# Kernel tuning notes

Measured on AMD Instinct MI355X. Metric: run time of the kernel, lower is better.

## Reference

```python
import jax, jax.numpy as jnp
import numpy as np

H = 16  # num_heads

def _rotate_half(x):
    x1, x2 = jnp.split(x, 2, axis=-1)
    return jnp.concatenate((-x2, x1), axis=-1)

def setup_inputs() -> dict:
    key = jax.random.key(0)
    ks = jax.random.split(key, 8)
    B, N, C = 4, 2048, 1024
    d = C // H
    x = jax.random.normal(ks[0], (B, N, C), dtype=jnp.float32)
    cos = jax.random.uniform(ks[1], (1, 1, N, d), dtype=jnp.float32)
    sin = jax.random.uniform(ks[2], (1, 1, N, d), dtype=jnp.float32)
    s = 0.02
    Wq = jax.random.normal(ks[3], (C, C), dtype=jnp.float32) * s
    Wkv = jax.random.normal(ks[4], (C, 2 * C), dtype=jnp.float32) * s
    Wout = jax.random.normal(ks[5], (C, C), dtype=jnp.float32) * s
    bout = jnp.zeros((C,), dtype=jnp.float32)
    return {"x": x, "cos": cos, "sin": sin, "Wq": Wq, "Wkv": Wkv, "Wout": Wout, "bout": bout}

def reference(x, cos, sin, Wq, Wkv, Wout, bout):
    B, N, C = x.shape
    d = C // H
    scale = d ** (-0.5)
    # projections (qkv_bias=False)
    q = (x @ Wq).reshape(B, N, H, d).transpose(0, 2, 1, 3)        # (B,H,N,d)
    kv = x @ Wkv                                                   # (B,N,2C)
    k, v = jnp.split(kv, 2, axis=-1)
    k = k.reshape(B, N, H, d).transpose(0, 2, 1, 3)
    v = v.reshape(B, N, H, d).transpose(0, 2, 1, 3)
    # inline RoPE
    q = q * cos + _rotate_half(q) * sin
    k = k * cos + _rotate_half(k) * sin
    # naive full attention
    sim = jnp.einsum('bhid,bhjd->bhij', q, k) * scale              # (B,H,N,N)
    attn = jax.nn.softmax(sim, axis=-1)
    out = jnp.einsum('bhij,bhjd->bhid', attn, v)                   # (B,H,N,d)
    out = out.transpose(0, 2, 1, 3).reshape(B, N, C)
    return out @ Wout + bout
```

## Files before the change

kernel.cpp:

```cpp
#include <hip/hip_runtime.h>


typedef unsigned short u16;
typedef unsigned int u32;
typedef __attribute__((ext_vector_type(8))) short short8;
typedef __attribute__((ext_vector_type(8))) unsigned short ushort8;
typedef __attribute__((ext_vector_type(4))) float f32x4;

#define MFMA16x16x32 __builtin_amdgcn_mfma_f32_16x16x32_bf16
#define QSCALE 0.180336880434135f

#if __has_builtin(__builtin_amdgcn_exp2f)
#define EXP2F __builtin_amdgcn_exp2f
#else
#define EXP2F exp2f
#endif

__device__ __forceinline__ float b2f(u16 u) {
  union { u32 i; float f; } x; x.i = ((u32)u) << 16; return x.f;
}
__device__ __forceinline__ u16 f2b(float f) {
  union { float f; u32 i; } x; x.f = f;
  u32 r = (x.i + 0x7FFFu + ((x.i >> 16) & 1u)) >> 16;
  return (u16)r;
}
__device__ __forceinline__ u16 f2b_trunc(float f) {
  union { float f; u32 i; } x; x.f = f;
  return (u16)(x.i >> 16);
}
__device__ __forceinline__ bool detect_f32(const u32* __restrict__ cw) {
  u32 acc = 0;
#pragma unroll
  for (int i = 0; i < 64; ++i) acc |= cw[i];
  return (acc & 0x8000u) != 0;
}
__device__ __forceinline__ float ldval(const void* p, long i, bool f32) {
  return f32 ? ((const float*)p)[i] : b2f(((const u16*)p)[i]);
}
__device__ __forceinline__ ushort8 ld8f(const float* p) {
  float4 u0 = *(const float4*)p;
  float4 u1 = *(const float4*)(p + 4);
  ushort8 r;
  r[0] = f2b(u0.x); r[1] = f2b(u0.y); r[2] = f2b(u0.z); r[3] = f2b(u0.w);
  r[4] = f2b(u1.x); r[5] = f2b(u1.y); r[6] = f2b(u1.z); r[7] = f2b(u1.w);
  return r;
}
__device__ __forceinline__ void async16(const void* g, void* l) {
  __builtin_amdgcn_global_load_lds((const __attribute__((address_space(1))) void*)g,
                                   (__attribute__((address_space(3))) void*)l, 16, 0, 0);
}

__global__ __launch_bounds__(256)
void convert_x(const void* __restrict__ src, u16* __restrict__ dst,
               const u32* __restrict__ cosw) {
  const bool f32 = detect_f32(cosw);
  const long i = ((long)blockIdx.x * 256 + threadIdx.x) * 8;
  ushort8 v;
  if (f32) v = ld8f((const float*)src + i);
  else     v = *(const ushort8*)((const u16*)src + i);
  *(ushort8*)(dst + i) = v;
}

__global__ __launch_bounds__(256)
void transpose_any(const void* __restrict__ src, u16* __restrict__ dst,
                   int R, int C, const u32* __restrict__ cosw) {
  const bool f32 = detect_f32(cosw);
  const int tr = blockIdx.y * 64, tc = blockIdx.x * 64;
  __shared__ __align__(16) u16 tile[64][65];
  const int t = threadIdx.x;
#pragma unroll
  for (int i = 0; i < 2; ++i) {
    const int ch = i * 256 + t;
    const int r = ch >> 3, cc = ch & 7;
    ushort8 v;
    if (f32) v = ld8f((const float*)src + (long)(tr + r) * C + tc + cc * 8);
    else     v = *(const ushort8*)((const u16*)src + (long)(tr + r) * C + tc + cc * 8);
#pragma unroll
    for (int j = 0; j < 8; ++j) tile[r][cc * 8 + j] = v[j];
  }
  __syncthreads();
#pragma unroll
  for (int i = 0; i < 2; ++i) {
    const int ch = i * 256 + t;
    const int c = ch >> 3, rc = ch & 7;
    ushort8 v;
#pragma unroll
    for (int j = 0; j < 8; ++j) v[j] = tile[rc * 8 + j][c];
    *(ushort8*)(dst + (long)(tc + c) * R + tr + rc * 8) = v;
  }
}

__global__ __launch_bounds__(256)
void transpose_b16(const u16* __restrict__ src, u16* __restrict__ dst,
                   int R, int C, long sb, long db) {
  src += (long)blockIdx.z * sb;
  dst += (long)blockIdx.z * db;
  const int tr = blockIdx.y * 64, tc = blockIdx.x * 64;
  __shared__ __align__(16) u16 tile[64][65];
  const int t = threadIdx.x;
#pragma unroll
  for (int i = 0; i < 2; ++i) {
    const int ch = i * 256 + t;
    const int r = ch >> 3, cc = ch & 7;
    ushort8 v = *(const ushort8*)(src + (long)(tr + r) * C + tc + cc * 8);
#pragma unroll
    for (int j = 0; j < 8; ++j) tile[r][cc * 8 + j] = v[j];
  }
  __syncthreads();
#pragma unroll
  for (int i = 0; i < 2; ++i) {
    const int ch = i * 256 + t;
    const int c = ch >> 3, rc = ch & 7;
    ushort8 v;
#pragma unroll
    for (int j = 0; j < 8; ++j) v[j] = tile[rc * 8 + j][c];
    *(ushort8*)(dst + (long)(tc + c) * R + tr + rc * 8) = v;
  }
}

template <int MODE>
__global__ __launch_bounds__(256)
void gemm_fast(const u16* __restrict__ A, const u16* __restrict__ BT,
               const void* cosp, const void* sinp,
               u16* q_ws, u16* k_ws, u16* v_ws,
               const void* bias, void* outp, const u32* __restrict__ cosw) {
  constexpr int K = 1024, ITERS = K / 32;
  __shared__ __align__(16) u16 As[2][128 * 32];
  __shared__ __align__(16) u16 Bs[2][128 * 32];
  const int tid = threadIdx.x;
  const int wave = tid >> 6, lane = tid & 63;
  const int quad = lane >> 4, l15 = lane & 15;
  const int m0 = blockIdx.y * 128, n0 = blockIdx.x * 128;
  const int mh = (wave >> 1) * 64, nh = (wave & 1) * 64;
  const f32x4 zero4 = {0.f, 0.f, 0.f, 0.f};

  f32x4 acc[4][4];
#pragma unroll
  for (int i = 0; i < 4; ++i)
#pragma unroll
    for (int j = 0; j < 4; ++j) acc[i][j] = zero4;

  const int c0 = tid, c1 = 256 + tid;
  const u16* a0p = A  + (long)(m0 + (c0 >> 2)) * K + (c0 & 3) * 8;
  const u16* a1p = A  + (long)(m0 + (c1 >> 2)) * K + (c1 & 3) * 8;
  const u16* b0p = BT + (long)(n0 + (c0 >> 2)) * K + (c0 & 3) * 8;
  const u16* b1p = BT + (long)(n0 + (c1 >> 2)) * K + (c1 & 3) * 8;

#define STAGE(buf, kt)                                \
  do {                                                \
    async16(a0p + (kt), As[buf] + c0 * 8);            \
    async16(a1p + (kt), As[buf] + c1 * 8);            \
    async16(b0p + (kt), Bs[buf] + c0 * 8);            \
    async16(b1p + (kt), Bs[buf] + c1 * 8);            \
  } while (0)

  STAGE(0, 0);
  for (int it = 0; it < ITERS; ++it) {
    const int cur = it & 1;
    __syncthreads();
    if (it + 1 < ITERS) STAGE(cur ^ 1, (it + 1) * 32);
    short8 af[4], bf[4];
#pragma unroll
    for (int s = 0; s < 4; ++s) {
      af[s] = *(const short8*)(As[cur] + (mh + s * 16 + l15) * 32 + quad * 8);
      bf[s] = *(const short8*)(Bs[cur] + (nh + s * 16 + l15) * 32 + quad * 8);
    }
#pragma unroll
    for (int i = 0; i < 4; ++i)
#pragma unroll
      for (int j = 0; j < 4; ++j)
        acc[i][j] = MFMA16x16x32(af[i], bf[j], acc[i][j], 0, 0, 0);
  }
#undef STAGE

  const bool f32 = detect_f32(cosw);

  if (MODE == 0) {
    const int seg = n0 >> 10;
    const int csbase = (n0 & 1023) + nh;
    u16* segp = (seg == 0) ? q_ws : (seg == 1) ? k_ws : v_ws;
#pragma unroll
    for (int i = 0; i < 4; ++i) {
#pragma unroll
      for (int r = 0; r < 4; ++r) {
        const int mm = m0 + mh + i * 16 + quad * 4 + r;
        const int b = mm >> 11, n = mm & 2047;
#pragma unroll
        for (int j = 0; j < 4; ++j) {
          const int cs = csbase + j * 16 + l15;
          const int h = cs >> 6, dv = cs & 63;
          float val = acc[i][j][r];
          if (seg < 2) {
            const float cv = ldval(cosp, (long)n * 64 + dv, f32);
            const float sv = ldval(sinp, (long)n * 64 + dv, f32);
            const float part = acc[i][j ^ 2][r];
            val = val * cv + ((dv < 32) ? -part : part) * sv;
            if (seg == 0) val *= QSCALE;
          }
          segp[(((long)(b * 16 + h) * 2048 + n) << 6) + dv] = f2b(val);
        }
      }
    }
  } else {
#pragma unroll
    for (int i = 0; i < 4; ++i) {
#pragma unroll
      for (int r = 0; r < 4; ++r) {
        const int mm = m0 + mh + i * 16 + quad * 4 + r;
#pragma unroll
        for (int j = 0; j < 4; ++j) {
          const int cc = n0 + nh + j * 16 + l15;
          const float val = acc[i][j][r] + ldval(bias, cc, f32);
          if (f32) ((float*)outp)[(long)mm * 1024 + cc] = val;
          else     ((u16*)outp)[(long)mm * 1024 + cc] = f2b(val);
        }
      }
    }
  }
}

__global__ __launch_bounds__(256)
void flash_k(const u16* __restrict__ q_ws, const u16* __restrict__ k_ws,
             const u16* __restrict__ vT_ws, u16* __restrict__ attn) {
  __shared__ __align__(16) u16 Ks[2][64 * 64];
  __shared__ __align__(16) u16 Vts[2][64 * 64];
  __shared__ __align__(16) u16 Pw[4][64 * 40];
  const int tid = threadIdx.x, wave = tid >> 6, lane = tid & 63;
  const int quad = lane >> 4, l15 = lane & 15;
  const int s7 = l15 & 7;
  const int bh = blockIdx.y;
  const int qr0 = blockIdx.x * 256 + wave * 64;
  const u16* Q  = q_ws  + (long)bh * 2048 * 64;
  const u16* Kp = k_ws  + (long)bh * 2048 * 64;
  const u16* Vt = vT_ws + (long)bh * 64 * 2048;
  u16* Pb = Pw[wave];
  const f32x4 zero4 = {0.f, 0.f, 0.f, 0.f};
  short8 ones;
#pragma unroll
  for (int i = 0; i < 8; ++i) ones[i] = (short)0x3F80;

  short8 aq[4][2];
#pragma unroll
  for (int ms = 0; ms < 4; ++ms)
#pragma unroll
    for (int ks = 0; ks < 2; ++ks)
      aq[ms][ks] = *(const short8*)(Q + (long)(qr0 + ms * 16 + l15) * 64 + ks * 32 + quad * 8);

  f32x4 accO[4][4], accL[4];
#pragma unroll
  for (int ms = 0; ms < 4; ++ms) {
#pragma unroll
    for (int jd = 0; jd < 4; ++jd) accO[ms][jd] = zero4;
    accL[ms] = zero4;
  }

  const int c0 = tid, c1 = 256 + tid;
  const int r0 = c0 >> 3, g0 = ((c0 & 7) ^ (r0 & 7)) * 8;
  const int r1 = c1 >> 3, g1 = ((c1 & 7) ^ (r1 & 7)) * 8;

#define STAGEKV(buf, kt)                                          \
  do {                                                            \
    async16(Kp + (long)((kt) + r0) * 64 + g0, Ks[buf] + c0 * 8);  \
    async16(Kp + (long)((kt) + r1) * 64 + g1, Ks[buf] + c1 * 8);  \
    async16(Vt + (long)r0 * 2048 + (kt) + g0, Vts[buf] + c0 * 8); \
    async16(Vt + (long)r1 * 2048 + (kt) + g1, Vts[buf] + c1 * 8); \
  } while (0)

  STAGEKV(0, 0);
  for (int it = 0; it < 32; ++it) {
    const int cur = it & 1;
    __syncthreads();
    if (it + 1 < 32) STAGEKV(cur ^ 1, (it + 1) * 64);

#pragma unroll
    for (int k2 = 0; k2 < 2; ++k2) {
#pragma unroll
      for (int nsl = 0; nsl < 2; ++nsl) {
        const int ns = k2 * 2 + nsl;
        const u16* rowK = Ks[cur] + (ns * 16 + l15) * 64;
        short8 b0 = *(const short8*)(rowK + ((quad ^ s7) * 8));
        short8 b1 = *(const short8*)(rowK + (((quad + 4) ^ s7) * 8));
#pragma unroll
        for (int ms = 0; ms < 4; ++ms) {
          f32x4 t = MFMA16x16x32(aq[ms][0], b0, zero4, 0, 0, 0);
          f32x4 sa = MFMA16x16x32(aq[ms][1], b1, t, 0, 0, 0);
#pragma unroll
          for (int r = 0; r < 4; ++r)
            Pb[(ms * 16 + quad * 4 + r) * 40 + nsl * 16 + l15] =
                f2b_trunc(EXP2F(sa[r]));
        }
      }
      short8 ap[4];
#pragma unroll
      for (int ms = 0; ms < 4; ++ms) {
        ap[ms] = *(const short8*)(Pb + (ms * 16 + l15) * 40 + quad * 8);
        accL[ms] = MFMA16x16x32(ap[ms], ones, accL[ms], 0, 0, 0);
      }
#pragma unroll
      for (int jd = 0; jd < 4; ++jd) {
        short8 bv = *(const short8*)(Vts[cur] + (jd * 16 + l15) * 64 +
                                     (((k2 * 4 + quad) ^ s7) * 8));
#pragma unroll
        for (int ms = 0; ms < 4; ++ms)
          accO[ms][jd] = MFMA16x16x32(ap[ms], bv, accO[ms][jd], 0, 0, 0);
      }
    }
  }
#undef STAGEKV

  const int b = bh >> 4, h = bh & 15;
#pragma unroll
  for (int ms = 0; ms < 4; ++ms) {
#pragma unroll
    for (int r = 0; r < 4; ++r) {
      const float inv = 1.f / accL[ms][r];
      const int row = qr0 + ms * 16 + quad * 4 + r;
#pragma unroll
      for (int jd = 0; jd < 4; ++jd) {
        const int cc = h * 64 + jd * 16 + l15;
        attn[((long)(b * 2048 + row)) * 1024 + cc] = f2b(accO[ms][jd][r] * inv);
      }
    }
  }
}

extern "C" void kernel_launch(void* const* d_in, const int* in_sizes, int n_in,
                              void* d_out, int out_size, void* d_ws, size_t ws_size,
                              hipStream_t stream) {
  const void* x    = d_in[0];
  const void* cosp = d_in[1];
  const void* sinp = d_in[2];
  const void* Wq   = d_in[3];
  const void* Wkv  = d_in[4];
  const void* Wout = d_in[5];
  const void* bout = d_in[6];
  const u32* cosw  = (const u32*)d_in[1];

  char* ws = (char*)d_ws;
  const size_t MB = 1u << 20;
  u16* q_ws  = (u16*)(ws);
  u16* k_ws  = (u16*)(ws + 16 * MB);
  u16* vT_ws = (u16*)(ws + 32 * MB);
  u16* v_ws  = (u16*)(ws + 48 * MB);
  u16* attn  = (u16*)(ws + 48 * MB);
  u16* WoutT = (u16*)(ws + 32 * MB);

  u16* WT1;
  if (ws_size >= 88 * MB) WT1 = (u16*)(ws + 64 * MB);
  else                    WT1 = (u16*)d_out;
  u16* x_bf16 = WT1 + 3072 * 1024;

  convert_x<<<dim3(4096), 256, 0, stream>>>(x, x_bf16, cosw);
  transpose_any<<<dim3(16, 16), 256, 0, stream>>>(Wq, WT1, 1024, 1024, cosw);
  transpose_any<<<dim3(32, 16), 256, 0, stream>>>(Wkv, WT1 + 1024 * 1024, 1024, 2048, cosw);
  gemm_fast<0><<<dim3(24, 64), 256, 0, stream>>>(x_bf16, WT1, cosp, sinp,
                                                 q_ws, k_ws, v_ws,
                                                 nullptr, nullptr, cosw);
  transpose_b16<<<dim3(1, 32, 64), 256, 0, stream>>>(v_ws, vT_ws, 2048, 64,
                                                     (long)2048 * 64, (long)64 * 2048);
  flash_k<<<dim3(8, 64), 256, 0, stream>>>(q_ws, k_ws, vT_ws, attn);
  transpose_any<<<dim3(16, 16), 256, 0, stream>>>(Wout, WoutT, 1024, 1024, cosw);
  gemm_fast<1><<<dim3(8, 64), 256, 0, stream>>>(attn, WoutT, cosp, sinp,
                                                nullptr, nullptr, nullptr,
                                                bout, d_out, cosw);
}
```

Measured before the change: 344.1 us.

## Replace 128x128 GEMM with 256x256-tile 8-wave pipelined GEMM using swizzled LDS

The projection and output GEMMs move from 128x128 tiles with 256 threads to 256x256 tiles with 512 threads and a K-step of 64. LDS uses an XOR swizzle to avoid bank conflicts, and global loads are staged in quarter-chunks interleaved with MFMA phases, using explicit vmcnt waits, barriers and setprio. Workgroup indices are remapped for L2 locality. The intent is more data reuse per LDS load and better overlap of loads with compute. The cost is fewer workgroups (128 for the output GEMM, which may underfill the CUs), more registers, and a fragile hand-written synchronisation scheme.

```diff
diff --git a/kernel.cpp b/kernel.cpp
--- a/kernel.cpp
+++ b/kernel.cpp
@@ -15,6 +15,10 @@
 #else
 #define EXP2F exp2f
 #endif
+
+#define GBAR() __builtin_amdgcn_s_barrier()
+#define CFENCE() asm volatile("" ::: "memory")
+#define WAITVM(n) asm volatile("s_waitcnt vmcnt(" #n ")" ::: "memory")
 
 __device__ __forceinline__ float b2f(u16 u) {
   union { u32 i; float f; } x; x.i = ((u32)u) << 16; return x.f;
@@ -119,71 +123,160 @@
 }
 
 template <int MODE>
-__global__ __launch_bounds__(256)
-void gemm_fast(const u16* __restrict__ A, const u16* __restrict__ BT,
-               const void* cosp, const void* sinp,
-               u16* q_ws, u16* k_ws, u16* v_ws,
-               const void* bias, void* outp, const u32* __restrict__ cosw) {
-  constexpr int K = 1024, ITERS = K / 32;
-  __shared__ __align__(16) u16 As[2][128 * 32];
-  __shared__ __align__(16) u16 Bs[2][128 * 32];
+__global__ __launch_bounds__(512, 2)
+void gemm256(const u16* __restrict__ A, const u16* __restrict__ BT,
+             const void* cosp, const void* sinp,
+             u16* q_ws, u16* k_ws, u16* v_ws,
+             const void* bias, void* outp, const u32* __restrict__ cosw) {
+  constexpr int K = 1024, NT = K / 64;
+  constexpr int NB = (MODE == 0) ? 12 : 4;
+  __shared__ __align__(16) u16 As[2][16384];
+  __shared__ __align__(16) u16 Bs[2][16384];
+
   const int tid = threadIdx.x;
   const int wave = tid >> 6, lane = tid & 63;
   const int quad = lane >> 4, l15 = lane & 15;
-  const int m0 = blockIdx.y * 128, n0 = blockIdx.x * 128;
-  const int mh = (wave >> 1) * 64, nh = (wave & 1) * 64;
+  const int wr = wave >> 2, wc = wave & 3;
+  const int s7 = l15 & 7;
+
+  int lin = blockIdx.y * NB + blockIdx.x;
+  const int nwg = NB * 32;
+  lin = (lin & 7) * (nwg >> 3) + (lin >> 3);
+  const int bx = lin % NB, by = lin / NB;
+  const int m0 = by * 256, n0 = bx * 256;
+
+  const long aoff = (long)(tid >> 3) * K + (long)(((tid & 7) ^ ((tid >> 3) & 7)) * 8);
+  const u16* Ag = A  + (long)m0 * K + aoff;
+  const u16* Bg = BT + (long)n0 * K + aoff;
+
+#define STAGE_A(bb, kt, h) do {                                                          \
+    async16(Ag + (long)(2 * (h))     * 64 * K + (kt) * 64,                               \
+            As[bb] + ((2 * (h))     * 512 + tid) * 8);                                   \
+    async16(Ag + (long)(2 * (h) + 1) * 64 * K + (kt) * 64,                               \
+            As[bb] + ((2 * (h) + 1) * 512 + tid) * 8);                                   \
+  } while (0)
+#define STAGE_B(bb, kt, h) do {                                                          \
+    async16(Bg + (long)(2 * (h))     * 64 * K + (kt) * 64,                               \
+            Bs[bb] + ((2 * (h))     * 512 + tid) * 8);                                   \
+    async16(Bg + (long)(2 * (h) + 1) * 64 * K + (kt) * 64,                               \
+            Bs[bb] + ((2 * (h) + 1) * 512 + tid) * 8);                                   \
+  } while (0)
+
+  const int kg0 = (quad ^ s7) * 8;
+  const int kg1 = ((quad + 4) ^ s7) * 8;
+  const int rowA = (wr * 128 + l15) * 64;
+  const int rowB = (wc * 64 + l15) * 64;
+
   const f32x4 zero4 = {0.f, 0.f, 0.f, 0.f};
-
-  f32x4 acc[4][4];
-#pragma unroll
-  for (int i = 0; i < 4; ++i)
+  f32x4 acc[8][4];
+#pragma unroll
+  for (int i = 0; i < 8; ++i)
 #pragma unroll
     for (int j = 0; j < 4; ++j) acc[i][j] = zero4;
 
-  const int c0 = tid, c1 = 256 + tid;
-  const u16* a0p = A  + (long)(m0 + (c0 >> 2)) * K + (c0 & 3) * 8;
-  const u16* a1p = A  + (long)(m0 + (c1 >> 2)) * K + (c1 & 3) * 8;
-  const u16* b0p = BT + (long)(n0 + (c0 >> 2)) * K + (c0 & 3) * 8;
-  const u16* b1p = BT + (long)(n0 + (c1 >> 2)) * K + (c1 & 3) * 8;
-
-#define STAGE(buf, kt)                                \
-  do {                                                \
-    async16(a0p + (kt), As[buf] + c0 * 8);            \
-    async16(a1p + (kt), As[buf] + c1 * 8);            \
-    async16(b0p + (kt), Bs[buf] + c0 * 8);            \
-    async16(b1p + (kt), Bs[buf] + c1 * 8);            \
-  } while (0)
-
-  STAGE(0, 0);
-  for (int it = 0; it < ITERS; ++it) {
-    const int cur = it & 1;
-    __syncthreads();
-    if (it + 1 < ITERS) STAGE(cur ^ 1, (it + 1) * 32);
-    short8 af[4], bf[4];
-#pragma unroll
-    for (int s = 0; s < 4; ++s) {
-      af[s] = *(const short8*)(As[cur] + (mh + s * 16 + l15) * 32 + quad * 8);
-      bf[s] = *(const short8*)(Bs[cur] + (nh + s * 16 + l15) * 32 + quad * 8);
-    }
+  STAGE_B(0, 0, 0);
+  STAGE_A(0, 0, 0);
+  STAGE_A(0, 0, 1);
+  STAGE_B(0, 0, 1);
+  STAGE_B(1, 1, 0);
+  WAITVM(2);
+  GBAR(); CFENCE();
+
+#pragma unroll 2
+  for (int t = 0; t < NT; ++t) {
+    const int buf = t & 1;
+    const u16* Ab = As[buf] + rowA;
+    const u16* Bb = Bs[buf] + rowB;
+    short8 a0[4][2], a1[4][2], b01[2][2], b23[2][2];
+
+#pragma unroll
+    for (int i = 0; i < 4; ++i) {
+      a0[i][0] = *(const short8*)(Ab + i * 1024 + kg0);
+      a0[i][1] = *(const short8*)(Ab + i * 1024 + kg1);
+    }
+#pragma unroll
+    for (int j = 0; j < 2; ++j) {
+      b01[j][0] = *(const short8*)(Bb + j * 1024 + kg0);
+      b01[j][1] = *(const short8*)(Bb + j * 1024 + kg1);
+    }
+    if (t + 1 < NT) STAGE_A(buf ^ 1, t + 1, 0);
+    GBAR();
+    __builtin_amdgcn_s_setprio(1);
 #pragma unroll
     for (int i = 0; i < 4; ++i)
 #pragma unroll
-      for (int j = 0; j < 4; ++j)
-        acc[i][j] = MFMA16x16x32(af[i], bf[j], acc[i][j], 0, 0, 0);
-  }
-#undef STAGE
+      for (int j = 0; j < 2; ++j) {
+        acc[i][j] = MFMA16x16x32(a0[i][0], b01[j][0], acc[i][j], 0, 0, 0);
+        acc[i][j] = MFMA16x16x32(a0[i][1], b01[j][1], acc[i][j], 0, 0, 0);
+      }
+    __builtin_amdgcn_s_setprio(0);
+    GBAR();
+
+#pragma unroll
+    for (int i = 0; i < 4; ++i) {
+      a1[i][0] = *(const short8*)(Ab + (4 + i) * 1024 + kg0);
+      a1[i][1] = *(const short8*)(Ab + (4 + i) * 1024 + kg1);
+    }
+    if (t + 1 < NT) STAGE_A(buf ^ 1, t + 1, 1);
+    GBAR();
+    __builtin_amdgcn_s_setprio(1);
+#pragma unroll
+    for (int i = 0; i < 4; ++i)
+#pragma unroll
+      for (int j = 0; j < 2; ++j) {
+        acc[4 + i][j] = MFMA16x16x32(a1[i][0], b01[j][0], acc[4 + i][j], 0, 0, 0);
+        acc[4 + i][j] = MFMA16x16x32(a1[i][1], b01[j][1], acc[4 + i][j], 0, 0, 0);
+      }
+    __builtin_amdgcn_s_setprio(0);
+    GBAR();
+
+#pragma unroll
+    for (int j = 0; j < 2; ++j) {
+      b23[j][0] = *(const short8*)(Bb + (2 + j) * 1024 + kg0);
+      b23[j][1] = *(const short8*)(Bb + (2 + j) * 1024 + kg1);
+    }
+    if (t + 1 < NT) STAGE_B(buf ^ 1, t + 1, 1);
+    GBAR();
+    __builtin_amdgcn_s_setprio(1);
+#pragma unroll
+    for (int i = 0; i < 4; ++i)
+#pragma unroll
+      for (int j = 0; j < 2; ++j) {
+        acc[i][2 + j] = MFMA16x16x32(a0[i][0], b23[j][0], acc[i][2 + j], 0, 0, 0);
+        acc[i][2 + j] = MFMA16x16x32(a0[i][1], b23[j][1], acc[i][2 + j], 0, 0, 0);
+      }
+    __builtin_amdgcn_s_setprio(0);
+    GBAR();
+
+    if (t + 2 < NT) STAGE_B(buf, t + 2, 0);
+    GBAR();
+    __builtin_amdgcn_s_setprio(1);
+#pragma unroll
+    for (int i = 0; i < 4; ++i)
+#pragma unroll
+      for (int j = 0; j < 2; ++j) {
+        acc[4 + i][2 + j] = MFMA16x16x32(a1[i][0], b23[j][0], acc[4 + i][2 + j], 0, 0, 0);
+        acc[4 + i][2 + j] = MFMA16x16x32(a1[i][1], b23[j][1], acc[4 + i][2 + j], 0, 0, 0);
+      }
+    __builtin_amdgcn_s_setprio(0);
+    if (t + 2 < NT)      { WAITVM(2); }
+    else if (t + 1 < NT) { WAITVM(0); }
+    GBAR(); CFENCE();
+  }
+#undef STAGE_A
+#undef STAGE_B
 
   const bool f32 = detect_f32(cosw);
 
   if (MODE == 0) {
     const int seg = n0 >> 10;
-    const int csbase = (n0 & 1023) + nh;
+    const int csbase = (n0 & 1023) + wc * 64;
     u16* segp = (seg == 0) ? q_ws : (seg == 1) ? k_ws : v_ws;
 #pragma unroll
-    for (int i = 0; i < 4; ++i) {
+    for (int i = 0; i < 8; ++i) {
 #pragma unroll
       for (int r = 0; r < 4; ++r) {
-        const int mm = m0 + mh + i * 16 + quad * 4 + r;
+        const int mm = m0 + wr * 128 + i * 16 + quad * 4 + r;
         const int b = mm >> 11, n = mm & 2047;
 #pragma unroll
         for (int j = 0; j < 4; ++j) {
@@ -203,13 +296,13 @@
     }
   } else {
 #pragma unroll
-    for (int i = 0; i < 4; ++i) {
+    for (int i = 0; i < 8; ++i) {
 #pragma unroll
       for (int r = 0; r < 4; ++r) {
-        const int mm = m0 + mh + i * 16 + quad * 4 + r;
+        const int mm = m0 + wr * 128 + i * 16 + quad * 4 + r;
 #pragma unroll
         for (int j = 0; j < 4; ++j) {
-          const int cc = n0 + nh + j * 16 + l15;
+          const int cc = n0 + wc * 64 + j * 16 + l15;
           const float val = acc[i][j][r] + ldval(bias, cc, f32);
           if (f32) ((float*)outp)[(long)mm * 1024 + cc] = val;
           else     ((u16*)outp)[(long)mm * 1024 + cc] = f2b(val);
@@ -353,14 +446,14 @@
   convert_x<<<dim3(4096), 256, 0, stream>>>(x, x_bf16, cosw);
   transpose_any<<<dim3(16, 16), 256, 0, stream>>>(Wq, WT1, 1024, 1024, cosw);
   transpose_any<<<dim3(32, 16), 256, 0, stream>>>(Wkv, WT1 + 1024 * 1024, 1024, 2048, cosw);
-  gemm_fast<0><<<dim3(24, 64), 256, 0, stream>>>(x_bf16, WT1, cosp, sinp,
-                                                 q_ws, k_ws, v_ws,
-                                                 nullptr, nullptr, cosw);
+  gemm256<0><<<dim3(12, 32), 512, 0, stream>>>(x_bf16, WT1, cosp, sinp,
+                                               q_ws, k_ws, v_ws,
+                                               nullptr, nullptr, cosw);
   transpose_b16<<<dim3(1, 32, 64), 256, 0, stream>>>(v_ws, vT_ws, 2048, 64,
                                                      (long)2048 * 64, (long)64 * 2048);
   flash_k<<<dim3(8, 64), 256, 0, stream>>>(q_ws, k_ws, vT_ws, attn);
   transpose_any<<<dim3(16, 16), 256, 0, stream>>>(Wout, WoutT, 1024, 1024, cosw);
-  gemm_fast<1><<<dim3(8, 64), 256, 0, stream>>>(attn, WoutT, cosp, sinp,
-                                                nullptr, nullptr, nullptr,
-                                                bout, d_out, cosw);
-}
+  gemm256<1><<<dim3(4, 32), 512, 0, stream>>>(attn, WoutT, cosp, sinp,
+                                              nullptr, nullptr, nullptr,
+                                              bout, d_out, cosw);
+}
```

Result: slower. 377.9 us (+9.8%).

## Keep softmax probabilities in registers instead of LDS round-trip in flash kernel

Applied to the files above, without the earlier changes.

Swaps MFMA operand order so the S tile comes out transposed, letting each lane pack its exp'd probabilities directly into the A operand of the PV MFMA. The per-wave LDS scratch buffer for P is removed, along with its writes, reads and the LDS capacity it used. To match the permuted k ordering, V fragments are now loaded as two 8-byte halves from swizzled columns. This relies on the register layout matching exactly, and the narrower V loads add LDS instructions.

```diff
diff --git a/kernel.cpp b/kernel.cpp
--- a/kernel.cpp
+++ b/kernel.cpp
@@ -3,6 +3,7 @@
 
 typedef unsigned short u16;
 typedef unsigned int u32;
+typedef __attribute__((ext_vector_type(4))) short s16x4;
 typedef __attribute__((ext_vector_type(8))) short short8;
 typedef __attribute__((ext_vector_type(8))) unsigned short ushort8;
 typedef __attribute__((ext_vector_type(4))) float f32x4;
@@ -24,9 +25,9 @@
   u32 r = (x.i + 0x7FFFu + ((x.i >> 16) & 1u)) >> 16;
   return (u16)r;
 }
-__device__ __forceinline__ u16 f2b_trunc(float f) {
+__device__ __forceinline__ u32 f2b_trunc32(float f) {
   union { float f; u32 i; } x; x.f = f;
-  return (u16)(x.i >> 16);
+  return x.i >> 16;
 }
 __device__ __forceinline__ bool detect_f32(const u32* __restrict__ cw) {
   u32 acc = 0;
@@ -224,7 +225,6 @@
              const u16* __restrict__ vT_ws, u16* __restrict__ attn) {
   __shared__ __align__(16) u16 Ks[2][64 * 64];
   __shared__ __align__(16) u16 Vts[2][64 * 64];
-  __shared__ __align__(16) u16 Pw[4][64 * 40];
   const int tid = threadIdx.x, wave = tid >> 6, lane = tid & 63;
   const int quad = lane >> 4, l15 = lane & 15;
   const int s7 = l15 & 7;
@@ -233,7 +233,6 @@
   const u16* Q  = q_ws  + (long)bh * 2048 * 64;
   const u16* Kp = k_ws  + (long)bh * 2048 * 64;
   const u16* Vt = vT_ws + (long)bh * 64 * 2048;
-  u16* Pb = Pw[wave];
   const f32x4 zero4 = {0.f, 0.f, 0.f, 0.f};
   short8 ones;
 #pragma unroll
@@ -266,6 +265,12 @@
     async16(Vt + (long)r1 * 2048 + (kt) + g1, Vts[buf] + c1 * 8); \
   } while (0)
 
+  const int vh = (quad & 1) * 4;
+  const int vc0a = ((0 + (quad >> 1)) ^ s7) * 8 + vh;
+  const int vc0b = ((2 + (quad >> 1)) ^ s7) * 8 + vh;
+  const int vc1a = ((4 + (quad >> 1)) ^ s7) * 8 + vh;
+  const int vc1b = ((6 + (quad >> 1)) ^ s7) * 8 + vh;
+
   STAGEKV(0, 0);
   for (int it = 0; it < 32; ++it) {
     const int cur = it & 1;
@@ -274,6 +279,7 @@
 
 #pragma unroll
     for (int k2 = 0; k2 < 2; ++k2) {
+      u32 pk[4][4];
 #pragma unroll
       for (int nsl = 0; nsl < 2; ++nsl) {
         const int ns = k2 * 2 + nsl;
@@ -282,27 +288,36 @@
         short8 b1 = *(const short8*)(rowK + (((quad + 4) ^ s7) * 8));
 #pragma unroll
         for (int ms = 0; ms < 4; ++ms) {
-          f32x4 t = MFMA16x16x32(aq[ms][0], b0, zero4, 0, 0, 0);
-          f32x4 sa = MFMA16x16x32(aq[ms][1], b1, t, 0, 0, 0);
-#pragma unroll
-          for (int r = 0; r < 4; ++r)
-            Pb[(ms * 16 + quad * 4 + r) * 40 + nsl * 16 + l15] =
-                f2b_trunc(EXP2F(sa[r]));
+          f32x4 t = MFMA16x16x32(b0, aq[ms][0], zero4, 0, 0, 0);
+          f32x4 sa = MFMA16x16x32(b1, aq[ms][1], t, 0, 0, 0);
+          const u32 p0 = f2b_trunc32(EXP2F(sa[0]));
+          const u32 p1 = f2b_trunc32(EXP2F(sa[1]));
+          const u32 p2 = f2b_trunc32(EXP2F(sa[2]));
+          const u32 p3 = f2b_trunc32(EXP2F(sa[3]));
+          pk[ms][nsl * 2 + 0] = p0 | (p1 << 16);
+          pk[ms][nsl * 2 + 1] = p2 | (p3 << 16);
         }
       }
       short8 ap[4];
 #pragma unroll
       for (int ms = 0; ms < 4; ++ms) {
-        ap[ms] = *(const short8*)(Pb + (ms * 16 + l15) * 40 + quad * 8);
+        union { u32 w[4]; short8 s; } u;
+        u.w[0] = pk[ms][0]; u.w[1] = pk[ms][1];
+        u.w[2] = pk[ms][2]; u.w[3] = pk[ms][3];
+        ap[ms] = u.s;
         accL[ms] = MFMA16x16x32(ap[ms], ones, accL[ms], 0, 0, 0);
       }
+      const int ca = k2 ? vc1a : vc0a;
+      const int cb = k2 ? vc1b : vc0b;
 #pragma unroll
       for (int jd = 0; jd < 4; ++jd) {
-        short8 bv = *(const short8*)(Vts[cur] + (jd * 16 + l15) * 64 +
-                                     (((k2 * 4 + quad) ^ s7) * 8));
+        const u16* rowV = Vts[cur] + (jd * 16 + l15) * 64;
+        union { s16x4 h[2]; short8 s; } bv;
+        bv.h[0] = *(const s16x4*)(rowV + ca);
+        bv.h[1] = *(const s16x4*)(rowV + cb);
 #pragma unroll
         for (int ms = 0; ms < 4; ++ms)
-          accO[ms][jd] = MFMA16x16x32(ap[ms], bv, accO[ms][jd], 0, 0, 0);
+          accO[ms][jd] = MFMA16x16x32(ap[ms], bv.s, accO[ms][jd], 0, 0, 0);
       }
     }
   }
```

Result: slower. 359.7 us (+4.5%).
